# Performance work log

Measured on AMD Instinct MI355X. Metric: run time of the kernel, lower is better.

The kernel has to match this reference:

```python
import jax, jax.numpy as jnp
import numpy as np

D_MODEL = 1024
N_HEADS = 16
D_K = D_MODEL // N_HEADS  # 64
B, T = 2, 2048


def setup_inputs() -> dict:
    key = jax.random.key(0)
    ks = jax.random.split(key, 6)
    s = 0.02
    x = jax.random.normal(ks[0], (B, T, D_MODEL), dtype=jnp.float32)
    # Stacked per-head projection weights, [H, C, d_k] (no bias, mini-gpt style)
    Wq = jax.random.normal(ks[1], (N_HEADS, D_MODEL, D_K), dtype=jnp.float32) * s
    Wk = jax.random.normal(ks[2], (N_HEADS, D_MODEL, D_K), dtype=jnp.float32) * s
    Wv = jax.random.normal(ks[3], (N_HEADS, D_MODEL, D_K), dtype=jnp.float32) * s
    # Output projection, torch nn.Linear(d_model, d_model): y = x @ Wo.T + bo
    Wo = jax.random.normal(ks[4], (D_MODEL, D_MODEL), dtype=jnp.float32) * s
    bo = jax.random.normal(ks[5], (D_MODEL,), dtype=jnp.float32) * s
    return {"x": x, "Wq": Wq, "Wk": Wk, "Wv": Wv, "Wo": Wo, "bo": bo}


def reference(x, Wq, Wk, Wv, Wo, bo):
    Bq, Tq, C = x.shape
    # Batched per-head projections (replaces the per-head Python loop)
    q = jnp.einsum('btc,hck->bhtk', x, Wq)  # [B,H,T,dk]
    k = jnp.einsum('btc,hck->bhtk', x, Wk)
    v = jnp.einsum('btc,hck->bhtk', x, Wv)
    scale = 1.0 / jnp.sqrt(jnp.asarray(D_K, dtype=x.dtype))
    scores = jnp.einsum('bhtk,bhsk->bhts', q, k) * scale  # [B,H,T,T]
    causal = jnp.tril(jnp.ones((Tq, Tq), dtype=bool))
    scores = jnp.where(causal, scores, jnp.asarray(-1e9, dtype=scores.dtype))
    attn = jax.nn.softmax(scores, axis=-1)
    out = jnp.einsum('bhts,bhsk->bhtk', attn, v)  # [B,H,T,dk]
    # concat heads -> [B,T,C]
    out = out.transpose(0, 2, 1, 3).reshape(Bq, Tq, C)
    return jnp.einsum('btc,dc->btd', out, Wo) + bo
```

## Files before the change

kernel.cpp:

```cpp
#include <hip/hip_runtime.h>
#include <hip/hip_bf16.h>


using short8 = __attribute__((ext_vector_type(8))) short;
using f32x4  = __attribute__((ext_vector_type(4))) float;
using fp16x2 = __attribute__((ext_vector_type(2))) __fp16;
using half4  = __attribute__((ext_vector_type(4))) _Float16;
using half8  = __attribute__((ext_vector_type(8))) _Float16;

#define SCALE_LOG2E 0.18033688011112042f

__device__ __forceinline__ unsigned short f2bf(float f) {
    union { float f; unsigned u; } v; v.f = f;
    unsigned r = v.u + 0x7fffu + ((v.u >> 16) & 1u);
    return (unsigned short)(r >> 16);
}

__device__ __forceinline__ void gld16(const unsigned short* gp, unsigned short* lp) {
    __builtin_amdgcn_global_load_lds(
        (const __attribute__((address_space(1))) void*)(gp),
        (__attribute__((address_space(3))) void*)(unsigned int)(unsigned long long)(lp),
        16, 0, 0);
}

__global__ void cvt_bf16(const float* __restrict__ in,
                         unsigned short* __restrict__ out, int n4) {
    int i = blockIdx.x * blockDim.x + threadIdx.x;
    if (i >= n4) return;
    float4 v = ((const float4*)in)[i];
    ushort4 o;
    o.x = f2bf(v.x); o.y = f2bf(v.y); o.z = f2bf(v.z); o.w = f2bf(v.w);
    ((ushort4*)out)[i] = o;
}

__global__ void transpose_w(const float* __restrict__ Wq,
                            const float* __restrict__ Wk,
                            const float* __restrict__ Wv,
                            unsigned short* __restrict__ out) {
    __shared__ float tile[64][65];
    int b = blockIdx.x;
    int cchunk = b & 15;
    int h = (b >> 4) & 15;
    int s = b >> 8;
    const float* W = (s == 0) ? Wq : ((s == 1) ? Wk : Wv);
    float sc = (s == 0) ? SCALE_LOG2E : 1.0f;
    const float* src = W + (h * 1024 + cchunk * 64) * 64;
    int t = threadIdx.x;
    #pragma unroll
    for (int it = 0; it < 4; ++it) {
        int idx = (it * 256 + t) * 4;
        int cc = idx >> 6, kk = idx & 63;
        float4 v = *(const float4*)(src + idx);
        tile[cc][kk + 0] = v.x; tile[cc][kk + 1] = v.y;
        tile[cc][kk + 2] = v.z; tile[cc][kk + 3] = v.w;
    }
    __syncthreads();
    unsigned short* dst = out + (size_t)((s * 16 + h) * 64) * 1024 + cchunk * 64;
    #pragma unroll
    for (int it = 0; it < 16; ++it) {
        int idx = it * 256 + t;
        int kk = idx >> 6, cc = idx & 63;
        dst[kk * 1024 + cc] = f2bf(tile[cc][kk] * sc);
    }
}

#define GEMM_CORE(A_, B_, m0_, n0_)                                          \
    __shared__ unsigned short Als[128 * 64];                                 \
    __shared__ unsigned short Bls[128 * 64];                                 \
    int wave = threadIdx.x >> 6;                                             \
    int lane = threadIdx.x & 63;                                             \
    int col  = lane & 15;                                                    \
    int quad = lane >> 4;                                                    \
    int m_off = (wave & 1) * 64;                                             \
    int n_off = (wave >> 1) * 64;                                            \
    int ldr = lane >> 3;                                                     \
    int ldc = ((lane & 7) ^ ldr) * 8;                                        \
    f32x4 acc[4][4] = {};                                                    \
    for (int k0 = 0; k0 < 1024; k0 += 64) {                                  \
        __syncthreads();                                                     \
        _Pragma("unroll")                                                    \
        for (int j = 0; j < 4; ++j) {                                        \
            int row = wave * 32 + j * 8;                                     \
            gld16(A_ + (size_t)(m0_ + row + ldr) * 1024 + k0 + ldc,          \
                  Als + row * 64);                                           \
            gld16(B_ + (size_t)(n0_ + row + ldr) * 1024 + k0 + ldc,          \
                  Bls + row * 64);                                           \
        }                                                                    \
        __syncthreads();                                                     \
        _Pragma("unroll")                                                    \
        for (int kh = 0; kh < 2; ++kh) {                                     \
            short8 af[4], bf[4];                                             \
            _Pragma("unroll")                                                \
            for (int i = 0; i < 4; ++i) {                                    \
                int lc = kh * 4 + quad;                                      \
                int sw = (lc ^ (col & 7)) * 8;                               \
                af[i] = *(const short8*)(Als + (m_off + i * 16 + col) * 64 + sw); \
                bf[i] = *(const short8*)(Bls + (n_off + i * 16 + col) * 64 + sw); \
            }                                                                \
            _Pragma("unroll")                                                \
            for (int mb = 0; mb < 4; ++mb)                                   \
                _Pragma("unroll")                                            \
                for (int nb = 0; nb < 4; ++nb)                               \
                    acc[mb][nb] = __builtin_amdgcn_mfma_f32_16x16x32_bf16(   \
                        af[mb], bf[nb], acc[mb][nb], 0, 0, 0);               \
        }                                                                    \
    }

__global__ __launch_bounds__(256) void qkv_gemm(
        const unsigned short* __restrict__ xb,
        const unsigned short* __restrict__ Wt,
        unsigned short* __restrict__ qB,
        unsigned short* __restrict__ kfrag,
        _Float16* __restrict__ vfrag) {
    int m0 = blockIdx.x * 128;
    int n0 = blockIdx.y * 128;
    GEMM_CORE(xb, Wt, m0, n0)
    int sel = blockIdx.y >> 3;
    #pragma unroll
    for (int nb = 0; nb < 4; ++nb) {
        int n = n0 + n_off + nb * 16 + col;
        int d10 = n & 1023;
        int h_ = d10 >> 6, d = d10 & 63;
        if (sel == 0) {
            #pragma unroll
            for (int mb = 0; mb < 4; ++mb)
                #pragma unroll
                for (int r = 0; r < 4; ++r) {
                    int m = m0 + m_off + mb * 16 + quad * 4 + r;
                    int b_ = m >> 11, t_ = m & 2047;
                    qB[((size_t)(b_ * 16 + h_) * 2048 + t_) * 64 + d] =
                        f2bf(acc[mb][nb][r]);
                }
        } else if (sel == 1) {
            int hK = d >> 5, quadk = (d >> 3) & 3, j = d & 7;
            #pragma unroll
            for (int mb = 0; mb < 4; ++mb)
                #pragma unroll
                for (int r = 0; r < 4; ++r) {
                    int m = m0 + m_off + mb * 16 + quad * 4 + r;
                    int b_ = m >> 11, t_ = m & 2047;
                    int bh = b_ * 16 + h_;
                    kfrag[((((size_t)bh * 128 + (t_ >> 4)) * 2 + hK) * 64 +
                           quadk * 16 + (t_ & 15)) * 8 + j] = f2bf(acc[mb][nb][r]);
                }
        } else {
            int nbv = d >> 4, colv = d & 15;
            #pragma unroll
            for (int mb = 0; mb < 4; ++mb) {
                int m = m0 + m_off + mb * 16 + quad * 4;
                int b_ = m >> 11, t_ = m & 2047;
                int bh = b_ * 16 + h_;
                half4 hv;
                hv[0] = (_Float16)acc[mb][nb][0]; hv[1] = (_Float16)acc[mb][nb][1];
                hv[2] = (_Float16)acc[mb][nb][2]; hv[3] = (_Float16)acc[mb][nb][3];
                *(half4*)(vfrag + ((((size_t)bh * 64 + (t_ >> 5)) * 4 + nbv) * 64 +
                          ((t_ >> 2) & 3) * 16 + colv) * 8 + ((t_ >> 4) & 1) * 4) = hv;
            }
        }
    }
}

__global__ __launch_bounds__(256) void oproj(
        const unsigned short* __restrict__ A,
        const unsigned short* __restrict__ Bw,
        const float* __restrict__ bo,
        float* __restrict__ y) {
    int m0 = blockIdx.x * 128;
    int n0 = blockIdx.y * 128;
    GEMM_CORE(A, Bw, m0, n0)
    #pragma unroll
    for (int nb = 0; nb < 4; ++nb) {
        int n = n0 + n_off + nb * 16 + col;
        float bias = bo[n];
        #pragma unroll
        for (int mb = 0; mb < 4; ++mb)
            #pragma unroll
            for (int r = 0; r < 4; ++r) {
                int m = m0 + m_off + mb * 16 + quad * 4 + r;
                y[(size_t)m * 1024 + n] = acc[mb][nb][r] + bias;
            }
    }
}

__global__ __launch_bounds__(256, 3) void attn(
        const unsigned short* __restrict__ qB,
        const unsigned short* __restrict__ kfrag,
        const _Float16* __restrict__ vfrag,
        unsigned short* __restrict__ aout) {
    __shared__ float O_comb[2][64][33];
    __shared__ float L_comb[2][2][2][16];
    int wave = threadIdx.x >> 6;
    int lane = threadIdx.x & 63;
    int col  = lane & 15;
    int quad = lane >> 4;
    int sl     = wave >> 1;
    int parity = wave & 1;
    int bh   = blockIdx.x & 31;
    int pairidx = 31 - (blockIdx.x >> 5);
    int strip = pairidx * 2 + sl;
    int q0 = strip * 32;
    const unsigned short* q = qB + (size_t)bh * 2048 * 64;
    const unsigned short* kf_base = kfrag + (size_t)bh * 128 * 2 * 512;
    const _Float16*       vf_base = vfrag + (size_t)bh * 64 * 4 * 512;

    short8 qf[2][2];
    #pragma unroll
    for (int qb = 0; qb < 2; ++qb)
        #pragma unroll
        for (int h = 0; h < 2; ++h)
            qf[qb][h] = *(const short8*)(q + (size_t)(q0 + qb * 16 + col) * 64 + h * 32 + quad * 8);

    f32x4 o[2][4] = {};
    float l[2] = {0.f, 0.f};

    struct KV { short8 kf[2][2]; half8 vv[4]; };
    KV bufA, bufB;

    auto load_half = [&](int it, int kv32, KV& b) {
        int K16 = it * 4 + kv32 * 2;
        #pragma unroll
        for (int p = 0; p < 2; ++p)
            #pragma unroll
            for (int h = 0; h < 2; ++h)
                b.kf[p][h] = *(const short8*)(kf_base +
                    (((size_t)(K16 + p) * 2 + h) * 64 + lane) * 8);
        #pragma unroll
        for (int nb = 0; nb < 4; ++nb)
            b.vv[nb] = *(const half8*)(vf_base +
                (((size_t)(it * 2 + kv32) * 4 + nb) * 64 + lane) * 8);
    };

    auto compute_half = [&](int it, int kv32, KV& b) {
        int kv0 = it * 64;
        bool diag = (kv0 + 63 > q0);
        #pragma unroll
        for (int par = 0; par < 2; ++par) {
            int kvbase = kv0 + kv32 * 32 + par * 16;
            f32x4 st[2] = {};
            #pragma unroll
            for (int qb = 0; qb < 2; ++qb) {
                st[qb] = __builtin_amdgcn_mfma_f32_16x16x32_bf16(b.kf[par][0], qf[qb][0], st[qb], 0, 0, 0);
                st[qb] = __builtin_amdgcn_mfma_f32_16x16x32_bf16(b.kf[par][1], qf[qb][1], st[qb], 0, 0, 0);
            }
            #pragma unroll
            for (int qb = 0; qb < 2; ++qb) {
                float p0 = __builtin_amdgcn_exp2f(st[qb][0]);
                float p1 = __builtin_amdgcn_exp2f(st[qb][1]);
                float p2 = __builtin_amdgcn_exp2f(st[qb][2]);
                float p3 = __builtin_amdgcn_exp2f(st[qb][3]);
                if (diag) {
                    int qg  = q0 + qb * 16 + col;
                    int kvg = kvbase + quad * 4;
                    p0 = (kvg + 0 > qg) ? 0.f : p0;
                    p1 = (kvg + 1 > qg) ? 0.f : p1;
                    p2 = (kvg + 2 > qg) ? 0.f : p2;
                    p3 = (kvg + 3 > qg) ? 0.f : p3;
                }
                l[qb] += (p0 + p1) + (p2 + p3);
                union { fp16x2 h2[2]; half4 h4; } cvt;
                cvt.h2[0] = __builtin_amdgcn_cvt_pkrtz(p0, p1);
                cvt.h2[1] = __builtin_amdgcn_cvt_pkrtz(p2, p3);
                half4 pf = cvt.h4;
                #pragma unroll
                for (int nb = 0; nb < 4; ++nb) {
                    half4 vf = (par == 0)
                        ? __builtin_shufflevector(b.vv[nb], b.vv[nb], 0, 1, 2, 3)
                        : __builtin_shufflevector(b.vv[nb], b.vv[nb], 4, 5, 6, 7);
                    o[qb][nb] = __builtin_amdgcn_mfma_f32_16x16x16f16(pf, vf, o[qb][nb], 0, 0, 0);
                }
            }
        }
    };

    int n_iter = (q0 + 95) >> 6;
    if (parity < n_iter) load_half(parity, 0, bufA);
    for (int it = parity; it < n_iter; it += 2) {
        load_half(it, 1, bufB);
        compute_half(it, 0, bufA);
        if (it + 2 < n_iter) load_half(it + 2, 0, bufA);
        compute_half(it, 1, bufB);
    }

    #pragma unroll
    for (int qb = 0; qb < 2; ++qb) {
        float lr = l[qb];
        lr += __shfl_xor(lr, 16);
        lr += __shfl_xor(lr, 32);
        l[qb] = lr;
    }
    if (quad == 0) {
        L_comb[sl][parity][0][col] = l[0];
        L_comb[sl][parity][1][col] = l[1];
    }
    if (parity == 1) {
        #pragma unroll
        for (int qb = 0; qb < 2; ++qb)
            #pragma unroll
            for (int nb = 0; nb < 4; ++nb)
                #pragma unroll
                for (int r = 0; r < 4; ++r)
                    O_comb[sl][lane][qb * 16 + nb * 4 + r] = o[qb][nb][r];
    }
    __syncthreads();
    if (parity == 0) {
        int b_ = bh >> 4, h_ = bh & 15;
        #pragma unroll
        for (int qb = 0; qb < 2; ++qb)
            #pragma unroll
            for (int r = 0; r < 4; ++r) {
                int qi = quad * 4 + r;
                float inv_l = 1.0f / (L_comb[sl][0][qb][qi] + L_comb[sl][1][qb][qi]);
                int t_ = q0 + qb * 16 + qi;
                #pragma unroll
                for (int nb = 0; nb < 4; ++nb) {
                    float ov = o[qb][nb][r] + O_comb[sl][lane][qb * 16 + nb * 4 + r];
                    aout[(size_t)(b_ * 2048 + t_) * 1024 + h_ * 64 + nb * 16 + col] =
                        f2bf(ov * inv_l);
                }
            }
    }
}

extern "C" void kernel_launch(void* const* d_in, const int* in_sizes, int n_in,
                              void* d_out, int out_size, void* d_ws, size_t ws_size,
                              hipStream_t stream) {
    const float* x  = (const float*)d_in[0];
    const float* Wq = (const float*)d_in[1];
    const float* Wk = (const float*)d_in[2];
    const float* Wv = (const float*)d_in[3];
    const float* Wo = (const float*)d_in[4];
    const float* bo = (const float*)d_in[5];
    float* y = (float*)d_out;

    unsigned short* xb    = (unsigned short*)d_ws;
    unsigned short* Wt    = xb    + 4194304;
    unsigned short* Wob   = Wt    + 3145728;
    unsigned short* qBb   = Wob   + 1048576;
    unsigned short* kfr   = qBb   + 4194304;
    unsigned short* vfr   = kfr   + 4194304;
    unsigned short* aout  = vfr   + 4194304;

    cvt_bf16<<<4096, 256, 0, stream>>>(x,  xb,  1048576);
    cvt_bf16<<<1024, 256, 0, stream>>>(Wo, Wob, 262144);
    transpose_w<<<768, 256, 0, stream>>>(Wq, Wk, Wv, Wt);
    qkv_gemm<<<dim3(32, 24), 256, 0, stream>>>(xb, Wt, qBb, kfr, (_Float16*)vfr);
    attn<<<1024, 256, 0, stream>>>(qBb, kfr, (const _Float16*)vfr, aout);
    oproj<<<dim3(32, 8), 256, 0, stream>>>(aout, Wob, bo, y);
}
```

Measured before the change: 182.0 us.

## Split attention KV across four waves per strip, shrink GEMM k-tile and oproj N-tile

The attention kernel now gives each block a single 32-row query strip and spreads the key/value loop over four waves instead of two. The partial O and L values are combined through shared memory, and the grid grows to 2048 blocks with launch bounds raised to 4 blocks per SM, aiming for more parallelism and occupancy. The shared GEMM core halves its k-tile to 32 with a new LDS swizzle, which cuts LDS use but doubles the barrier count. The output projection gets its own kernel with 64-wide N tiles and twice as many blocks, to fill more CUs.

```diff
diff --git a/kernel.cpp b/kernel.cpp
--- a/kernel.cpp
+++ b/kernel.cpp
@@ -65,45 +65,41 @@
 }
 
 #define GEMM_CORE(A_, B_, m0_, n0_)                                          \
-    __shared__ unsigned short Als[128 * 64];                                 \
-    __shared__ unsigned short Bls[128 * 64];                                 \
+    __shared__ unsigned short Als[128 * 32];                                 \
+    __shared__ unsigned short Bls[128 * 32];                                 \
     int wave = threadIdx.x >> 6;                                             \
     int lane = threadIdx.x & 63;                                             \
     int col  = lane & 15;                                                    \
     int quad = lane >> 4;                                                    \
     int m_off = (wave & 1) * 64;                                             \
     int n_off = (wave >> 1) * 64;                                            \
-    int ldr = lane >> 3;                                                     \
-    int ldc = ((lane & 7) ^ ldr) * 8;                                        \
+    int ldr = lane >> 2;                                                     \
+    int ldc = ((lane & 3) ^ ((lane >> 3) & 3)) * 8;                          \
+    int swq = (quad ^ ((col >> 1) & 3)) * 8;                                 \
     f32x4 acc[4][4] = {};                                                    \
-    for (int k0 = 0; k0 < 1024; k0 += 64) {                                  \
+    for (int k0 = 0; k0 < 1024; k0 += 32) {                                  \
         __syncthreads();                                                     \
         _Pragma("unroll")                                                    \
-        for (int j = 0; j < 4; ++j) {                                        \
-            int row = wave * 32 + j * 8;                                     \
+        for (int j = 0; j < 2; ++j) {                                        \
+            int row = wave * 32 + j * 16;                                    \
             gld16(A_ + (size_t)(m0_ + row + ldr) * 1024 + k0 + ldc,          \
-                  Als + row * 64);                                           \
+                  Als + row * 32);                                           \
             gld16(B_ + (size_t)(n0_ + row + ldr) * 1024 + k0 + ldc,          \
-                  Bls + row * 64);                                           \
+                  Bls + row * 32);                                           \
         }                                                                    \
         __syncthreads();                                                     \
+        short8 af[4], bf[4];                                                 \
         _Pragma("unroll")                                                    \
-        for (int kh = 0; kh < 2; ++kh) {                                     \
-            short8 af[4], bf[4];                                             \
+        for (int i = 0; i < 4; ++i) {                                        \
+            af[i] = *(const short8*)(Als + (m_off + i * 16 + col) * 32 + swq); \
+            bf[i] = *(const short8*)(Bls + (n_off + i * 16 + col) * 32 + swq); \
+        }                                                                    \
+        _Pragma("unroll")                                                    \
+        for (int mb = 0; mb < 4; ++mb)                                       \
             _Pragma("unroll")                                                \
-            for (int i = 0; i < 4; ++i) {                                    \
-                int lc = kh * 4 + quad;                                      \
-                int sw = (lc ^ (col & 7)) * 8;                               \
-                af[i] = *(const short8*)(Als + (m_off + i * 16 + col) * 64 + sw); \
-                bf[i] = *(const short8*)(Bls + (n_off + i * 16 + col) * 64 + sw); \
-            }                                                                \
-            _Pragma("unroll")                                                \
-            for (int mb = 0; mb < 4; ++mb)                                   \
-                _Pragma("unroll")                                            \
-                for (int nb = 0; nb < 4; ++nb)                               \
-                    acc[mb][nb] = __builtin_amdgcn_mfma_f32_16x16x32_bf16(   \
-                        af[mb], bf[nb], acc[mb][nb], 0, 0, 0);               \
-        }                                                                    \
+            for (int nb = 0; nb < 4; ++nb)                                   \
+                acc[mb][nb] = __builtin_amdgcn_mfma_f32_16x16x32_bf16(       \
+                    af[mb], bf[nb], acc[mb][nb], 0, 0, 0);                   \
     }
 
 __global__ __launch_bounds__(256) void qkv_gemm(
@@ -165,11 +161,48 @@
         const unsigned short* __restrict__ Bw,
         const float* __restrict__ bo,
         float* __restrict__ y) {
+    __shared__ unsigned short Als[128 * 32];
+    __shared__ unsigned short Bls[64 * 32];
+    int wave = threadIdx.x >> 6;
+    int lane = threadIdx.x & 63;
+    int col  = lane & 15;
+    int quad = lane >> 4;
+    int m_off = (wave & 1) * 64;
+    int n_off = (wave >> 1) * 32;
+    int ldr = lane >> 2;
+    int ldc = ((lane & 3) ^ ((lane >> 3) & 3)) * 8;
+    int swq = (quad ^ ((col >> 1) & 3)) * 8;
     int m0 = blockIdx.x * 128;
-    int n0 = blockIdx.y * 128;
-    GEMM_CORE(A, Bw, m0, n0)
-    #pragma unroll
-    for (int nb = 0; nb < 4; ++nb) {
+    int n0 = blockIdx.y * 64;
+    f32x4 acc[4][2] = {};
+    for (int k0 = 0; k0 < 1024; k0 += 32) {
+        __syncthreads();
+        #pragma unroll
+        for (int j = 0; j < 2; ++j) {
+            int row = wave * 32 + j * 16;
+            gld16(A + (size_t)(m0 + row + ldr) * 1024 + k0 + ldc, Als + row * 32);
+        }
+        {
+            int row = wave * 16;
+            gld16(Bw + (size_t)(n0 + row + ldr) * 1024 + k0 + ldc, Bls + row * 32);
+        }
+        __syncthreads();
+        short8 af[4], bf[2];
+        #pragma unroll
+        for (int i = 0; i < 4; ++i)
+            af[i] = *(const short8*)(Als + (m_off + i * 16 + col) * 32 + swq);
+        #pragma unroll
+        for (int i = 0; i < 2; ++i)
+            bf[i] = *(const short8*)(Bls + (n_off + i * 16 + col) * 32 + swq);
+        #pragma unroll
+        for (int mb = 0; mb < 4; ++mb)
+            #pragma unroll
+            for (int nb = 0; nb < 2; ++nb)
+                acc[mb][nb] = __builtin_amdgcn_mfma_f32_16x16x32_bf16(
+                    af[mb], bf[nb], acc[mb][nb], 0, 0, 0);
+    }
+    #pragma unroll
+    for (int nb = 0; nb < 2; ++nb) {
         int n = n0 + n_off + nb * 16 + col;
         float bias = bo[n];
         #pragma unroll
@@ -182,22 +215,19 @@
     }
 }
 
-__global__ __launch_bounds__(256, 3) void attn(
+__global__ __launch_bounds__(256, 4) void attn(
         const unsigned short* __restrict__ qB,
         const unsigned short* __restrict__ kfrag,
         const _Float16* __restrict__ vfrag,
         unsigned short* __restrict__ aout) {
-    __shared__ float O_comb[2][64][33];
-    __shared__ float L_comb[2][2][2][16];
-    int wave = threadIdx.x >> 6;
+    __shared__ float O_comb[3][64][33];
+    __shared__ float L_comb[4][2][16];
+    int parity = threadIdx.x >> 6;
     int lane = threadIdx.x & 63;
     int col  = lane & 15;
     int quad = lane >> 4;
-    int sl     = wave >> 1;
-    int parity = wave & 1;
-    int bh   = blockIdx.x & 31;
-    int pairidx = 31 - (blockIdx.x >> 5);
-    int strip = pairidx * 2 + sl;
+    int bh    = blockIdx.x & 31;
+    int strip = 63 - (blockIdx.x >> 5);
     int q0 = strip * 32;
     const unsigned short* q = qB + (size_t)bh * 2048 * 64;
     const unsigned short* kf_base = kfrag + (size_t)bh * 128 * 2 * 512;
@@ -273,12 +303,14 @@
     };
 
     int n_iter = (q0 + 95) >> 6;
-    if (parity < n_iter) load_half(parity, 0, bufA);
-    for (int it = parity; it < n_iter; it += 2) {
-        load_half(it, 1, bufB);
-        compute_half(it, 0, bufA);
-        if (it + 2 < n_iter) load_half(it + 2, 0, bufA);
-        compute_half(it, 1, bufB);
+    if (parity < n_iter) {
+        load_half(parity, 0, bufA);
+        for (int it = parity; it < n_iter; it += 4) {
+            load_half(it, 1, bufB);
+            compute_half(it, 0, bufA);
+            if (it + 4 < n_iter) load_half(it + 4, 0, bufA);
+            compute_half(it, 1, bufB);
+        }
     }
 
     #pragma unroll
@@ -289,17 +321,17 @@
         l[qb] = lr;
     }
     if (quad == 0) {
-        L_comb[sl][parity][0][col] = l[0];
-        L_comb[sl][parity][1][col] = l[1];
-    }
-    if (parity == 1) {
+        L_comb[parity][0][col] = l[0];
+        L_comb[parity][1][col] = l[1];
+    }
+    if (parity > 0) {
         #pragma unroll
         for (int qb = 0; qb < 2; ++qb)
             #pragma unroll
             for (int nb = 0; nb < 4; ++nb)
                 #pragma unroll
                 for (int r = 0; r < 4; ++r)
-                    O_comb[sl][lane][qb * 16 + nb * 4 + r] = o[qb][nb][r];
+                    O_comb[parity - 1][lane][qb * 16 + nb * 4 + r] = o[qb][nb][r];
     }
     __syncthreads();
     if (parity == 0) {
@@ -309,11 +341,14 @@
             #pragma unroll
             for (int r = 0; r < 4; ++r) {
                 int qi = quad * 4 + r;
-                float inv_l = 1.0f / (L_comb[sl][0][qb][qi] + L_comb[sl][1][qb][qi]);
+                float inv_l = 1.0f / (L_comb[0][qb][qi] + L_comb[1][qb][qi] +
+                                      L_comb[2][qb][qi] + L_comb[3][qb][qi]);
                 int t_ = q0 + qb * 16 + qi;
                 #pragma unroll
                 for (int nb = 0; nb < 4; ++nb) {
-                    float ov = o[qb][nb][r] + O_comb[sl][lane][qb * 16 + nb * 4 + r];
+                    float ov = o[qb][nb][r] + O_comb[0][lane][qb * 16 + nb * 4 + r]
+                                            + O_comb[1][lane][qb * 16 + nb * 4 + r]
+                                            + O_comb[2][lane][qb * 16 + nb * 4 + r];
                     aout[(size_t)(b_ * 2048 + t_) * 1024 + h_ * 64 + nb * 16 + col] =
                         f2bf(ov * inv_l);
                 }
@@ -344,6 +379,6 @@
     cvt_bf16<<<1024, 256, 0, stream>>>(Wo, Wob, 262144);
     transpose_w<<<768, 256, 0, stream>>>(Wq, Wk, Wv, Wt);
     qkv_gemm<<<dim3(32, 24), 256, 0, stream>>>(xb, Wt, qBb, kfr, (_Float16*)vfr);
-    attn<<<1024, 256, 0, stream>>>(qBb, kfr, (const _Float16*)vfr, aout);
-    oproj<<<dim3(32, 8), 256, 0, stream>>>(aout, Wob, bo, y);
-}
+    attn<<<2048, 256, 0, stream>>>(qBb, kfr, (const _Float16*)vfr, aout);
+    oproj<<<dim3(32, 16), 256, 0, stream>>>(aout, Wob, bo, y);
+}
```

Result: slower. 300.5 us (+65.1%).
